# Optimization experiments

Measured on AMD Instinct MI355X. Metric: run time of the kernel, lower is better.

The kernel has to match this reference:

```python
import jax, jax.numpy as jnp
import numpy as np

N_NODES = 100000
N_FEAT = 128
HIDDEN = 64
N_CLASSES = 40
N_EDGES = 1600000


def gcn_conv(x, W, b, src, dst, n):
    # x: [N, F_in], W: [F_in, F_out]. GCNConv: linear, then sym-normalized aggregation, then bias.
    h = x @ W  # [N, F_out]
    deg = jax.ops.segment_sum(jnp.ones_like(dst, dtype=h.dtype), dst, num_segments=n)  # in-degree incl self-loops
    dinv = jnp.where(deg > 0, jax.lax.rsqrt(deg), 0.0)
    norm = dinv[src] * dinv[dst]  # [E']
    msg = h[src] * norm[:, None]  # gather + scale
    out = jax.ops.segment_sum(msg, dst, num_segments=n)  # scatter-add into targets
    return out + b


def add_self_loops(edge_index, n):
    loops = jnp.arange(n, dtype=edge_index.dtype)
    src = jnp.concatenate([edge_index[0], loops])
    dst = jnp.concatenate([edge_index[1], loops])
    return src, dst


def setup_inputs() -> dict:
    key = jax.random.key(0)
    k1, k2, k3, k4, k5, k6 = jax.random.split(key, 6)
    x = jax.random.normal(k1, (N_NODES, N_FEAT), dtype=jnp.float32)
    edge_index = jax.random.randint(k2, (2, N_EDGES), 0, N_NODES, dtype=jnp.int32)
    # Glorot init like PyG GCNConv
    W1 = jax.random.normal(k3, (N_FEAT, HIDDEN), dtype=jnp.float32) * (2.0 / (N_FEAT + HIDDEN)) ** 0.5
    b1 = jnp.zeros((HIDDEN,), dtype=jnp.float32)
    W2 = jax.random.normal(k4, (HIDDEN, N_CLASSES), dtype=jnp.float32) * (2.0 / (HIDDEN + N_CLASSES)) ** 0.5
    b2 = jnp.zeros((N_CLASSES,), dtype=jnp.float32)
    return {"x": x, "edge_index": edge_index, "W1": W1, "b1": b1, "W2": W2, "b2": b2}


def reference(x, edge_index, W1, b1, W2, b2):
    n = x.shape[0]
    src, dst = add_self_loops(edge_index, n)
    h = jax.nn.relu(gcn_conv(x, W1, b1, src, dst, n))
    # F.dropout with training=False (eval mode) is identity
    out = gcn_conv(h, W2, b2, src, dst, n)
    return out
```

## Files before the change

### kernel.cpp

```cpp
#include <hip/hip_runtime.h>
#include <hip/hip_fp16.h>


#define NPB 256
#define NB_MAX 512
#define NCH 256
#define SCAN_BLK 1024

typedef _Float16 f16;
typedef f16 f16x8 __attribute__((ext_vector_type(8)));
typedef float f32x4 __attribute__((ext_vector_type(4)));

__global__ __launch_bounds__(256) void k_hist(const int* __restrict__ dst, int* __restrict__ ghist,
                                              int E, int NB, int chunk) {
    __shared__ int h[NB_MAX];
    int tid = threadIdx.x, w = blockIdx.x;
    for (int b = tid; b < NB; b += 256) h[b] = 0;
    __syncthreads();
    int beg = w * chunk, end = min(E, beg + chunk);
    for (int e = beg + tid; e < end; e += 256) atomicAdd(&h[dst[e] >> 8], 1);
    __syncthreads();
    for (int b = tid; b < NB; b += 256) ghist[b * NCH + w] = h[b];
}

__global__ __launch_bounds__(256) void k_scan_reduce(const int* __restrict__ ghist, int* __restrict__ wsum, int M) {
    __shared__ int s[256];
    int tid = threadIdx.x;
    int base = blockIdx.x * SCAN_BLK + tid * 4;
    int v = 0;
    if (base + 3 < M) {
        int4 r = *reinterpret_cast<const int4*>(&ghist[base]);
        v = r.x + r.y + r.z + r.w;
    } else {
        for (int j = 0; j < 4; ++j) if (base + j < M) v += ghist[base + j];
    }
    s[tid] = v;
    __syncthreads();
    for (int off = 128; off > 0; off >>= 1) {
        if (tid < off) s[tid] += s[tid + off];
        __syncthreads();
    }
    if (tid == 0) wsum[blockIdx.x] = s[0];
}

__global__ __launch_bounds__(128) void k_scan_mid(int* __restrict__ wsum, int* __restrict__ bucketBase,
                                                  int nw, int NB, int E) {
    __shared__ int s[128];
    int tid = threadIdx.x;
    int v = (tid < nw) ? wsum[tid] : 0;
    s[tid] = v;
    __syncthreads();
    for (int off = 1; off < 128; off <<= 1) {
        int add = (tid >= off) ? s[tid - off] : 0;
        __syncthreads();
        s[tid] += add;
        __syncthreads();
    }
    if (tid < nw) wsum[tid] = s[tid] - v;
    if (tid == 0) bucketBase[NB] = E;
}

__global__ __launch_bounds__(256) void k_scan_apply(const int* __restrict__ ghist, const int* __restrict__ wsum,
                                                    int* __restrict__ gbase, int* __restrict__ bucketBase, int M) {
    __shared__ int s[256];
    int tid = threadIdx.x;
    int base = blockIdx.x * SCAN_BLK + tid * 4;
    int e[4];
    int v = 0;
#pragma unroll
    for (int j = 0; j < 4; ++j) {
        int val = (base + j < M) ? ghist[base + j] : 0;
        e[j] = v;
        v += val;
    }
    s[tid] = v;
    __syncthreads();
    for (int off = 1; off < 256; off <<= 1) {
        int add = (tid >= off) ? s[tid - off] : 0;
        __syncthreads();
        s[tid] += add;
        __syncthreads();
    }
    int tbase = wsum[blockIdx.x] + s[tid] - v;
#pragma unroll
    for (int j = 0; j < 4; ++j) {
        int i = base + j;
        if (i < M) {
            int g = tbase + e[j];
            gbase[i] = g;
            if ((i & (NCH - 1)) == 0) bucketBase[i / NCH] = g;
        }
    }
}

__global__ __launch_bounds__(256) void k_partition(const int* __restrict__ src, const int* __restrict__ dst,
                                                   const int* __restrict__ gbase, unsigned int* __restrict__ ebuf,
                                                   int E, int NB, int chunk) {
    __shared__ int cur[NB_MAX];
    int tid = threadIdx.x, w = blockIdx.x;
    for (int b = tid; b < NB; b += 256) cur[b] = gbase[b * NCH + w];
    __syncthreads();
    int beg = w * chunk, end = min(E, beg + chunk);
    for (int e = beg + tid; e < end; e += 256) {
        int d = dst[e];
        int b = d >> 8;
        int pos = atomicAdd(&cur[b], 1);
        ebuf[pos] = (unsigned int)src[e] | ((unsigned int)(d & 255) << 24);
    }
}

__global__ __launch_bounds__(256) void k_csr(const unsigned int* __restrict__ ebuf,
                                             const int* __restrict__ bucketBase,
                                             int* __restrict__ rowptr, float* __restrict__ dinv,
                                             int* __restrict__ csr, int n, int E) {
    __shared__ int cnt[NPB];
    __shared__ int sc[NPB];
    __shared__ int cur[NPB];
    int tid = threadIdx.x, b = blockIdx.x;
    int ebeg = bucketBase[b], eend = bucketBase[b + 1];
    cnt[tid] = 0;
    __syncthreads();
    for (int i = ebeg + tid; i < eend; i += 256) atomicAdd(&cnt[ebuf[i] >> 24], 1);
    __syncthreads();
    int v = cnt[tid];
    sc[tid] = v;
    __syncthreads();
    for (int off = 1; off < 256; off <<= 1) {
        int add = (tid >= off) ? sc[tid - off] : 0;
        __syncthreads();
        sc[tid] += add;
        __syncthreads();
    }
    int ex = sc[tid] - v;
    cur[tid] = ex;
    int node = b * NPB + tid;
    if (node < n) {
        rowptr[node] = ebeg + ex;
        dinv[node] = rsqrtf((float)(v + 1));
    }
    if (b == 0 && tid == 0) rowptr[n] = E;
    __syncthreads();
    for (int i = ebeg + tid; i < eend; i += 256) {
        unsigned int word = ebuf[i];
        int pos = atomicAdd(&cur[word >> 24], 1);
        csr[ebeg + pos] = (int)(word & 0xFFFFFFu);
    }
}

__global__ __launch_bounds__(256) void k_gemm1(const float* __restrict__ x, const float* __restrict__ W1,
                                               const float* __restrict__ dinv, __half* __restrict__ g1,
                                               int n) {
    __shared__ f16 Wt[64][136];
    int tid = threadIdx.x;
    for (int i = tid; i < 128 * 64; i += 256) {
        int k = i >> 6, c = i & 63;
        Wt[c][k] = (f16)W1[i];
    }
    __syncthreads();

    int wv = tid >> 6, lane = tid & 63;
    int lrow = lane & 15, lk = (lane >> 4) * 8;
    int drow0 = (lane >> 4) * 4, dcol = lane & 15;

    int ntile = (n + 63) >> 6;
    for (int rg = blockIdx.x; rg < ntile; rg += gridDim.x) {
        int arow = rg * 64 + wv * 16 + lrow;
        f16x8 afrag[4];
        if (arow < n) {
            const float* xp = x + (size_t)arow * 128 + lk;
#pragma unroll
            for (int m = 0; m < 4; ++m) {
                float4 lo = *reinterpret_cast<const float4*>(xp + m * 32);
                float4 hi = *reinterpret_cast<const float4*>(xp + m * 32 + 4);
                f16x8 a;
                a[0] = (f16)lo.x; a[1] = (f16)lo.y; a[2] = (f16)lo.z; a[3] = (f16)lo.w;
                a[4] = (f16)hi.x; a[5] = (f16)hi.y; a[6] = (f16)hi.z; a[7] = (f16)hi.w;
                afrag[m] = a;
            }
        } else {
#pragma unroll
            for (int m = 0; m < 4; ++m) afrag[m] = (f16x8)(f16)0.f;
        }
        f32x4 accs[4];
#pragma unroll
        for (int t = 0; t < 4; ++t) {
            f32x4 acc = {0.f, 0.f, 0.f, 0.f};
#pragma unroll
            for (int m = 0; m < 4; ++m) {
                f16x8 b = *reinterpret_cast<const f16x8*>(&Wt[t * 16 + lrow][m * 32 + lk]);
                acc = __builtin_amdgcn_mfma_f32_16x16x32_f16(afrag[m], b, acc, 0, 0, 0);
            }
            accs[t] = acc;
        }
#pragma unroll
        for (int r = 0; r < 4; ++r) {
            int grow = rg * 64 + wv * 16 + drow0 + r;
            if (grow < n) {
                float dd = dinv[grow];
#pragma unroll
                for (int t = 0; t < 4; ++t)
                    g1[(size_t)grow * 64 + t * 16 + dcol] = __float2half_rn(accs[t][r] * dd);
            }
        }
    }
}

__device__ __forceinline__ void acc_half4(float4& acc, uint2 r) {
    __half2 h0 = *reinterpret_cast<__half2*>(&r.x);
    __half2 h1 = *reinterpret_cast<__half2*>(&r.y);
    float2 f0 = __half22float2(h0);
    float2 f1 = __half22float2(h1);
    acc.x += f0.x; acc.y += f0.y; acc.z += f1.x; acc.w += f1.y;
}

__device__ __forceinline__ void acc_half8(float* acc, uint4 r) {
    const __half2* h = reinterpret_cast<const __half2*>(&r);
#pragma unroll
    for (int j = 0; j < 4; ++j) {
        float2 f = __half22float2(h[j]);
        acc[2 * j]     += f.x;
        acc[2 * j + 1] += f.y;
    }
}

__global__ __launch_bounds__(256) void k_agg1(const __half* __restrict__ g1, const int* __restrict__ rowptr,
                                              const int* __restrict__ csr, const float* __restrict__ dinv,
                                              float* __restrict__ agg1, int n) {
    int lane = threadIdx.x & 63;
    int v = blockIdx.x * 4 + (threadIdx.x >> 6);
    if (v >= n) return;
    int beg = rowptr[v], end = rowptr[v + 1];
    int sub = lane >> 3, fl = lane & 7;
    float acc[8] = {};
    int i = beg + sub;
    int s0 = (i < end) ? csr[i] : -1;
    int s1 = (i + 8 < end) ? csr[i + 8] : -1;
    while (s0 >= 0) {
        uint4 r0 = *reinterpret_cast<const uint4*>(&g1[(size_t)s0 * 64 + fl * 8]);
        uint4 r1;
        bool h1 = (s1 >= 0);
        if (h1) r1 = *reinterpret_cast<const uint4*>(&g1[(size_t)s1 * 64 + fl * 8]);
        i += 16;
        s0 = (i < end) ? csr[i] : -1;
        s1 = (i + 8 < end) ? csr[i + 8] : -1;
        acc_half8(acc, r0);
        if (h1) acc_half8(acc, r1);
    }
#pragma unroll
    for (int off = 8; off < 64; off <<= 1)
#pragma unroll
        for (int j = 0; j < 8; ++j) acc[j] += __shfl_xor(acc[j], off);
    if (sub == 0) {
        float self[8] = {};
        acc_half8(self, *reinterpret_cast<const uint4*>(&g1[(size_t)v * 64 + fl * 8]));
        float d = dinv[v];
        float4 o0, o1;
        o0.x = (acc[0] + self[0]) * d; o0.y = (acc[1] + self[1]) * d;
        o0.z = (acc[2] + self[2]) * d; o0.w = (acc[3] + self[3]) * d;
        o1.x = (acc[4] + self[4]) * d; o1.y = (acc[5] + self[5]) * d;
        o1.z = (acc[6] + self[6]) * d; o1.w = (acc[7] + self[7]) * d;
        *reinterpret_cast<float4*>(&agg1[(size_t)v * 64 + fl * 8]) = o0;
        *reinterpret_cast<float4*>(&agg1[(size_t)v * 64 + fl * 8 + 4]) = o1;
    }
}

__global__ __launch_bounds__(256) void k_gemm2(const float* __restrict__ agg1, const float* __restrict__ W2,
                                               const float* __restrict__ b1, const float* __restrict__ dinv,
                                               __half* __restrict__ g2, int n) {
    __shared__ float Ws[64 * 40];
    __shared__ float xs[32][65];
    int tid = threadIdx.x;
    for (int i = tid; i < 64 * 40; i += 256) Ws[i] = W2[i];
    int nrg = n >> 5;
    int r = tid >> 3, cb = (tid & 7) * 5;
    for (int rg = blockIdx.x; rg < nrg; rg += gridDim.x) {
        __syncthreads();
        int row0 = rg << 5;
        for (int i = tid; i < 32 * 64; i += 256) {
            int rr = i >> 6, k = i & 63;
            float vv = agg1[(row0 + rr) * 64 + k] + b1[k];
            xs[rr][k] = vv > 0.f ? vv : 0.f;
        }
        __syncthreads();
        float acc[5] = {0.f, 0.f, 0.f, 0.f, 0.f};
#pragma unroll
        for (int k = 0; k < 64; ++k) {
            float xv = xs[r][k];
#pragma unroll
            for (int j = 0; j < 5; ++j) acc[j] += xv * Ws[k * 40 + cb + j];
        }
        int row = row0 + r;
        float di = dinv[row];
#pragma unroll
        for (int j = 0; j < 5; ++j) g2[(size_t)row * 40 + cb + j] = __float2half_rn(acc[j] * di);
    }
}

__global__ __launch_bounds__(256) void k_agg2(const __half* __restrict__ g2, const int* __restrict__ rowptr,
                                              const int* __restrict__ csr, const float* __restrict__ dinv,
                                              const float* __restrict__ b2, float* __restrict__ out, int n) {
    int lane = threadIdx.x & 63;
    int v = blockIdx.x * 4 + (threadIdx.x >> 6);
    if (v >= n) return;
    int beg = rowptr[v], end = rowptr[v + 1];
    int sub = lane >> 4, fl = lane & 15;
    float4 acc = {0.f, 0.f, 0.f, 0.f};
    if (fl < 10) {
        int i = beg + sub;
        int s0 = (i < end) ? csr[i] : -1;
        int s1 = (i + 4 < end) ? csr[i + 4] : -1;
        while (s0 >= 0) {
            uint2 r0 = *reinterpret_cast<const uint2*>(&g2[(size_t)s0 * 40 + fl * 4]);
            uint2 r1;
            bool h1 = (s1 >= 0);
            if (h1) r1 = *reinterpret_cast<const uint2*>(&g2[(size_t)s1 * 40 + fl * 4]);
            i += 8;
            s0 = (i < end) ? csr[i] : -1;
            s1 = (i + 4 < end) ? csr[i + 4] : -1;
            acc_half4(acc, r0);
            if (h1) acc_half4(acc, r1);
        }
    }
#pragma unroll
    for (int off = 16; off < 64; off <<= 1) {
        acc.x += __shfl_xor(acc.x, off);
        acc.y += __shfl_xor(acc.y, off);
        acc.z += __shfl_xor(acc.z, off);
        acc.w += __shfl_xor(acc.w, off);
    }
    if (sub == 0 && fl < 10) {
        float4 self = {0.f, 0.f, 0.f, 0.f};
        acc_half4(self, *reinterpret_cast<const uint2*>(&g2[(size_t)v * 40 + fl * 4]));
        float4 bb = *reinterpret_cast<const float4*>(&b2[fl * 4]);
        float d = dinv[v];
        float4 o;
        o.x = (acc.x + self.x) * d + bb.x;
        o.y = (acc.y + self.y) * d + bb.y;
        o.z = (acc.z + self.z) * d + bb.z;
        o.w = (acc.w + self.w) * d + bb.w;
        *reinterpret_cast<float4*>(&out[(size_t)v * 40 + fl * 4]) = o;
    }
}

extern "C" void kernel_launch(void* const* d_in, const int* in_sizes, int n_in,
                              void* d_out, int out_size, void* d_ws, size_t ws_size,
                              hipStream_t stream) {
    const float* x  = (const float*)d_in[0];
    const int*   ei = (const int*)d_in[1];
    const float* W1 = (const float*)d_in[2];
    const float* b1 = (const float*)d_in[3];
    const float* W2 = (const float*)d_in[4];
    const float* b2 = (const float*)d_in[5];
    float* out = (float*)d_out;

    int N = in_sizes[0] / 128;
    int E = in_sizes[1] / 2;
    const int* src = ei;
    const int* dst = ei + E;

    int NB = (N + NPB - 1) / NPB;
    int chunk = (E + NCH - 1) / NCH;
    int M = NB * NCH;
    int nw = (M + SCAN_BLK - 1) / SCAN_BLK;

    char* w = (char*)d_ws;
    int*   ghist      = (int*)w;           w += (size_t)M * 4;
    int*   gbase      = (int*)w;           w += (size_t)M * 4;
    int*   bucketBase = (int*)w;           w += (size_t)(NB + 1) * 4 + 252;
    int*   wsum       = (int*)w;           w += 128 * 4;
    unsigned int* ebuf = (unsigned int*)w; w += (size_t)E * 4;
    int*   rowptr     = (int*)w;           w += (size_t)(N + 1) * 4 + 252;
    float* dinv       = (float*)w;         w += (size_t)N * 4 + 256;
    int*   csr        = (int*)w;           w += (size_t)E * 4;
    __half* g1        = (__half*)w;        w += (size_t)N * 64 * 2;
    float* agg1       = (float*)w;         w += (size_t)N * 64 * 4;
    __half* g2        = (__half*)w;

    k_hist<<<NCH, 256, 0, stream>>>(dst, ghist, E, NB, chunk);
    k_scan_reduce<<<nw, 256, 0, stream>>>(ghist, wsum, M);
    k_scan_mid<<<1, 128, 0, stream>>>(wsum, bucketBase, nw, NB, E);
    k_scan_apply<<<nw, 256, 0, stream>>>(ghist, wsum, gbase, bucketBase, M);
    k_partition<<<NCH, 256, 0, stream>>>(src, dst, gbase, ebuf, E, NB, chunk);
    k_csr<<<NB, 256, 0, stream>>>(ebuf, bucketBase, rowptr, dinv, csr, N, E);

    k_gemm1<<<1024, 256, 0, stream>>>(x, W1, dinv, g1, N);
    k_agg1<<<(N + 3) / 4, 256, 0, stream>>>(g1, rowptr, csr, dinv, agg1, N);
    k_gemm2<<<1024, 256, 0, stream>>>(agg1, W2, b1, dinv, g2, N);
    k_agg2<<<(N + 3) / 4, 256, 0, stream>>>(g2, rowptr, csr, dinv, b2, out, N);
}
```

Measured before the change: 284.6 us.

## Store layer-1 aggregate in fp16, pad g2 rows to 64, deepen gather unroll

The layer-1 aggregation output is written as fp16 instead of fp32, which halves the traffic between agg1 and gemm2. The g2 buffer is padded to 64 halves per row with zero-filled tail columns, so the layer-2 aggregation can reuse the same 16-byte-per-lane gather pattern as layer 1. Both aggregation loops now keep four neighbour loads in flight instead of two, for more memory-level parallelism. The trade-offs are extra fp16 rounding on the intermediate, about 60% more gathered bytes per edge in layer 2 from the padding, and higher register pressure.

```diff
diff --git a/kernel.cpp b/kernel.cpp
--- a/kernel.cpp
+++ b/kernel.cpp
@@ -205,15 +205,7 @@
     }
 }
 
-__device__ __forceinline__ void acc_half4(float4& acc, uint2 r) {
-    __half2 h0 = *reinterpret_cast<__half2*>(&r.x);
-    __half2 h1 = *reinterpret_cast<__half2*>(&r.y);
-    float2 f0 = __half22float2(h0);
-    float2 f1 = __half22float2(h1);
-    acc.x += f0.x; acc.y += f0.y; acc.z += f1.x; acc.w += f1.y;
-}
-
-__device__ __forceinline__ void acc_half8(float* acc, uint4 r) {
+__device__ __forceinline__ void acc_u4(float* acc, uint4 r) {
     const __half2* h = reinterpret_cast<const __half2*>(&r);
 #pragma unroll
     for (int j = 0; j < 4; ++j) {
@@ -225,26 +217,35 @@
 
 __global__ __launch_bounds__(256) void k_agg1(const __half* __restrict__ g1, const int* __restrict__ rowptr,
                                               const int* __restrict__ csr, const float* __restrict__ dinv,
-                                              float* __restrict__ agg1, int n) {
+                                              __half* __restrict__ agg1h, int n) {
     int lane = threadIdx.x & 63;
     int v = blockIdx.x * 4 + (threadIdx.x >> 6);
     if (v >= n) return;
     int beg = rowptr[v], end = rowptr[v + 1];
     int sub = lane >> 3, fl = lane & 7;
+    const __half* gb = g1 + (size_t)fl * 8;
     float acc[8] = {};
     int i = beg + sub;
-    int s0 = (i < end) ? csr[i] : -1;
-    int s1 = (i + 8 < end) ? csr[i + 8] : -1;
+    int s0 = (i      < end) ? csr[i]      : -1;
+    int s1 = (i + 8  < end) ? csr[i + 8]  : -1;
+    int s2 = (i + 16 < end) ? csr[i + 16] : -1;
+    int s3 = (i + 24 < end) ? csr[i + 24] : -1;
     while (s0 >= 0) {
-        uint4 r0 = *reinterpret_cast<const uint4*>(&g1[(size_t)s0 * 64 + fl * 8]);
-        uint4 r1;
-        bool h1 = (s1 >= 0);
-        if (h1) r1 = *reinterpret_cast<const uint4*>(&g1[(size_t)s1 * 64 + fl * 8]);
-        i += 16;
-        s0 = (i < end) ? csr[i] : -1;
-        s1 = (i + 8 < end) ? csr[i + 8] : -1;
-        acc_half8(acc, r0);
-        if (h1) acc_half8(acc, r1);
+        uint4 r0, r1, r2, r3;
+        bool h1 = s1 >= 0, h2 = s2 >= 0, h3 = s3 >= 0;
+        r0 = *reinterpret_cast<const uint4*>(&gb[(size_t)s0 * 64]);
+        if (h1) r1 = *reinterpret_cast<const uint4*>(&gb[(size_t)s1 * 64]);
+        if (h2) r2 = *reinterpret_cast<const uint4*>(&gb[(size_t)s2 * 64]);
+        if (h3) r3 = *reinterpret_cast<const uint4*>(&gb[(size_t)s3 * 64]);
+        i += 32;
+        s0 = (i      < end) ? csr[i]      : -1;
+        s1 = (i + 8  < end) ? csr[i + 8]  : -1;
+        s2 = (i + 16 < end) ? csr[i + 16] : -1;
+        s3 = (i + 24 < end) ? csr[i + 24] : -1;
+        acc_u4(acc, r0);
+        if (h1) acc_u4(acc, r1);
+        if (h2) acc_u4(acc, r2);
+        if (h3) acc_u4(acc, r3);
     }
 #pragma unroll
     for (int off = 8; off < 64; off <<= 1)
@@ -252,34 +253,46 @@
         for (int j = 0; j < 8; ++j) acc[j] += __shfl_xor(acc[j], off);
     if (sub == 0) {
         float self[8] = {};
-        acc_half8(self, *reinterpret_cast<const uint4*>(&g1[(size_t)v * 64 + fl * 8]));
+        acc_u4(self, *reinterpret_cast<const uint4*>(&gb[(size_t)v * 64]));
         float d = dinv[v];
-        float4 o0, o1;
-        o0.x = (acc[0] + self[0]) * d; o0.y = (acc[1] + self[1]) * d;
-        o0.z = (acc[2] + self[2]) * d; o0.w = (acc[3] + self[3]) * d;
-        o1.x = (acc[4] + self[4]) * d; o1.y = (acc[5] + self[5]) * d;
-        o1.z = (acc[6] + self[6]) * d; o1.w = (acc[7] + self[7]) * d;
-        *reinterpret_cast<float4*>(&agg1[(size_t)v * 64 + fl * 8]) = o0;
-        *reinterpret_cast<float4*>(&agg1[(size_t)v * 64 + fl * 8 + 4]) = o1;
-    }
-}
-
-__global__ __launch_bounds__(256) void k_gemm2(const float* __restrict__ agg1, const float* __restrict__ W2,
+        unsigned uu[4];
+#pragma unroll
+        for (int j = 0; j < 4; ++j) {
+            __half2 p = __floats2half2_rn((acc[2 * j] + self[2 * j]) * d,
+                                          (acc[2 * j + 1] + self[2 * j + 1]) * d);
+            uu[j] = *reinterpret_cast<unsigned*>(&p);
+        }
+        uint4 wq = {uu[0], uu[1], uu[2], uu[3]};
+        *reinterpret_cast<uint4*>(&agg1h[(size_t)v * 64 + fl * 8]) = wq;
+    }
+}
+
+__global__ __launch_bounds__(256) void k_gemm2(const __half* __restrict__ agg1h, const float* __restrict__ W2,
                                                const float* __restrict__ b1, const float* __restrict__ dinv,
                                                __half* __restrict__ g2, int n) {
     __shared__ float Ws[64 * 40];
+    __shared__ float b1s[64];
     __shared__ float xs[32][65];
     int tid = threadIdx.x;
     for (int i = tid; i < 64 * 40; i += 256) Ws[i] = W2[i];
+    if (tid < 64) b1s[tid] = b1[tid];
     int nrg = n >> 5;
     int r = tid >> 3, cb = (tid & 7) * 5;
     for (int rg = blockIdx.x; rg < nrg; rg += gridDim.x) {
         __syncthreads();
         int row0 = rg << 5;
-        for (int i = tid; i < 32 * 64; i += 256) {
-            int rr = i >> 6, k = i & 63;
-            float vv = agg1[(row0 + rr) * 64 + k] + b1[k];
-            xs[rr][k] = vv > 0.f ? vv : 0.f;
+        {
+            int rr = tid >> 3, part = (tid & 7) * 8;
+            uint4 rv = *reinterpret_cast<const uint4*>(&agg1h[(size_t)(row0 + rr) * 64 + part]);
+            const __half2* hp = reinterpret_cast<const __half2*>(&rv);
+#pragma unroll
+            for (int jj = 0; jj < 4; ++jj) {
+                float2 f = __half22float2(hp[jj]);
+                float v0 = f.x + b1s[part + 2 * jj];
+                float v1 = f.y + b1s[part + 2 * jj + 1];
+                xs[rr][part + 2 * jj]     = v0 > 0.f ? v0 : 0.f;
+                xs[rr][part + 2 * jj + 1] = v1 > 0.f ? v1 : 0.f;
+            }
         }
         __syncthreads();
         float acc[5] = {0.f, 0.f, 0.f, 0.f, 0.f};
@@ -292,7 +305,11 @@
         int row = row0 + r;
         float di = dinv[row];
 #pragma unroll
-        for (int j = 0; j < 5; ++j) g2[(size_t)row * 40 + cb + j] = __float2half_rn(acc[j] * di);
+        for (int j = 0; j < 5; ++j) g2[(size_t)row * 64 + cb + j] = __float2half_rn(acc[j] * di);
+        for (int i = tid; i < 32 * 24; i += 256) {
+            int rr = i / 24, c = 40 + i - (i / 24) * 24;
+            g2[(size_t)(row0 + rr) * 64 + c] = __float2half_rn(0.f);
+        }
     }
 }
 
@@ -303,42 +320,46 @@
     int v = blockIdx.x * 4 + (threadIdx.x >> 6);
     if (v >= n) return;
     int beg = rowptr[v], end = rowptr[v + 1];
-    int sub = lane >> 4, fl = lane & 15;
-    float4 acc = {0.f, 0.f, 0.f, 0.f};
-    if (fl < 10) {
-        int i = beg + sub;
-        int s0 = (i < end) ? csr[i] : -1;
-        int s1 = (i + 4 < end) ? csr[i + 4] : -1;
-        while (s0 >= 0) {
-            uint2 r0 = *reinterpret_cast<const uint2*>(&g2[(size_t)s0 * 40 + fl * 4]);
-            uint2 r1;
-            bool h1 = (s1 >= 0);
-            if (h1) r1 = *reinterpret_cast<const uint2*>(&g2[(size_t)s1 * 40 + fl * 4]);
-            i += 8;
-            s0 = (i < end) ? csr[i] : -1;
-            s1 = (i + 4 < end) ? csr[i + 4] : -1;
-            acc_half4(acc, r0);
-            if (h1) acc_half4(acc, r1);
-        }
-    }
-#pragma unroll
-    for (int off = 16; off < 64; off <<= 1) {
-        acc.x += __shfl_xor(acc.x, off);
-        acc.y += __shfl_xor(acc.y, off);
-        acc.z += __shfl_xor(acc.z, off);
-        acc.w += __shfl_xor(acc.w, off);
-    }
-    if (sub == 0 && fl < 10) {
-        float4 self = {0.f, 0.f, 0.f, 0.f};
-        acc_half4(self, *reinterpret_cast<const uint2*>(&g2[(size_t)v * 40 + fl * 4]));
-        float4 bb = *reinterpret_cast<const float4*>(&b2[fl * 4]);
+    int sub = lane >> 3, fl = lane & 7;
+    const __half* gb = g2 + (size_t)fl * 8;
+    float acc[8] = {};
+    int i = beg + sub;
+    int s0 = (i      < end) ? csr[i]      : -1;
+    int s1 = (i + 8  < end) ? csr[i + 8]  : -1;
+    int s2 = (i + 16 < end) ? csr[i + 16] : -1;
+    int s3 = (i + 24 < end) ? csr[i + 24] : -1;
+    while (s0 >= 0) {
+        uint4 r0, r1, r2, r3;
+        bool h1 = s1 >= 0, h2 = s2 >= 0, h3 = s3 >= 0;
+        r0 = *reinterpret_cast<const uint4*>(&gb[(size_t)s0 * 64]);
+        if (h1) r1 = *reinterpret_cast<const uint4*>(&gb[(size_t)s1 * 64]);
+        if (h2) r2 = *reinterpret_cast<const uint4*>(&gb[(size_t)s2 * 64]);
+        if (h3) r3 = *reinterpret_cast<const uint4*>(&gb[(size_t)s3 * 64]);
+        i += 32;
+        s0 = (i      < end) ? csr[i]      : -1;
+        s1 = (i + 8  < end) ? csr[i + 8]  : -1;
+        s2 = (i + 16 < end) ? csr[i + 16] : -1;
+        s3 = (i + 24 < end) ? csr[i + 24] : -1;
+        acc_u4(acc, r0);
+        if (h1) acc_u4(acc, r1);
+        if (h2) acc_u4(acc, r2);
+        if (h3) acc_u4(acc, r3);
+    }
+#pragma unroll
+    for (int off = 8; off < 64; off <<= 1)
+#pragma unroll
+        for (int j = 0; j < 8; ++j) acc[j] += __shfl_xor(acc[j], off);
+    if (sub == 0 && fl < 5) {
+        float self[8] = {};
+        acc_u4(self, *reinterpret_cast<const uint4*>(&gb[(size_t)v * 64]));
         float d = dinv[v];
-        float4 o;
-        o.x = (acc.x + self.x) * d + bb.x;
-        o.y = (acc.y + self.y) * d + bb.y;
-        o.z = (acc.z + self.z) * d + bb.z;
-        o.w = (acc.w + self.w) * d + bb.w;
-        *reinterpret_cast<float4*>(&out[(size_t)v * 40 + fl * 4]) = o;
+        float o[8];
+#pragma unroll
+        for (int j = 0; j < 8; ++j) o[j] = (acc[j] + self[j]) * d + b2[fl * 8 + j];
+        float4 o0 = {o[0], o[1], o[2], o[3]};
+        float4 o1 = {o[4], o[5], o[6], o[7]};
+        *reinterpret_cast<float4*>(&out[(size_t)v * 40 + fl * 8]) = o0;
+        *reinterpret_cast<float4*>(&out[(size_t)v * 40 + fl * 8 + 4]) = o1;
     }
 }
 
@@ -373,7 +394,7 @@
     float* dinv       = (float*)w;         w += (size_t)N * 4 + 256;
     int*   csr        = (int*)w;           w += (size_t)E * 4;
     __half* g1        = (__half*)w;        w += (size_t)N * 64 * 2;
-    float* agg1       = (float*)w;         w += (size_t)N * 64 * 4;
+    __half* agg1h     = (__half*)w;        w += (size_t)N * 64 * 2;
     __half* g2        = (__half*)w;
 
     k_hist<<<NCH, 256, 0, stream>>>(dst, ghist, E, NB, chunk);
@@ -384,7 +405,7 @@
     k_csr<<<NB, 256, 0, stream>>>(ebuf, bucketBase, rowptr, dinv, csr, N, E);
 
     k_gemm1<<<1024, 256, 0, stream>>>(x, W1, dinv, g1, N);
-    k_agg1<<<(N + 3) / 4, 256, 0, stream>>>(g1, rowptr, csr, dinv, agg1, N);
-    k_gemm2<<<1024, 256, 0, stream>>>(agg1, W2, b1, dinv, g2, N);
+    k_agg1<<<(N + 3) / 4, 256, 0, stream>>>(g1, rowptr, csr, dinv, agg1h, N);
+    k_gemm2<<<1024, 256, 0, stream>>>(agg1h, W2, b1, dinv, g2, N);
     k_agg2<<<(N + 3) / 4, 256, 0, stream>>>(g2, rowptr, csr, dinv, b2, out, N);
 }
```

New measurement: 286.7 us. No clear change (+0.7%).
